# Kernel tuning notes

Hardware: AMD Instinct MI355X
Metric: run time of the kernel (lower is better)

The kernel has to match this reference:

```python
import jax, jax.numpy as jnp
from jax import lax
import numpy as np

B, CG, CY, H, W = 4, 384, 2, 224, 224
CH = 32  # gate / hidden channel count


def conv2d_same(x, w):
    # x: [B,C,H,W], w: [O,I,3,3], stride 1, padding 1, no bias
    return lax.conv_general_dilated(x, w, (1, 1), ((1, 1), (1, 1)),
                                    dimension_numbers=("NCHW", "OIHW", "NCHW"))


def norm_gates(g1, g2, g3):
    # torch: normalize by sum_abs only where sum_abs >= 1, else keep raw gates.
    # Equivalent to dividing by max(sum_abs, 1).
    denom = jnp.maximum(jnp.abs(g1) + jnp.abs(g2) + jnp.abs(g3), 1.0)
    return g1 / denom, g2 / denom, g3 / denom


def propagate(x, g1, g2, g3, horizontal, reverse):
    # GateRecurrent2dnoind: serial scan along W (horizontal) or H (vertical).
    # h(t) = (1 - g1 - g2 - g3) * x(t) + g1*h_prev(i-1) + g2*h_prev(i) + g3*h_prev(i+1)
    ax = 3 if horizontal else 2

    def prep(a):
        a = jnp.flip(a, ax) if reverse else a
        return jnp.moveaxis(a, ax, 0)  # [T, B, C, S]

    xs = (prep(x), prep(g1), prep(g2), prep(g3))

    def step(h, inp):
        xt, a1, a2, a3 = inp
        hu = jnp.pad(h, ((0, 0), (0, 0), (1, 0)))[:, :, :-1]  # neighbor i-1
        hd = jnp.pad(h, ((0, 0), (0, 0), (0, 1)))[:, :, 1:]   # neighbor i+1
        h = (1.0 - a1 - a2 - a3) * xt + a1 * hu + a2 * h + a3 * hd
        return h, h

    h0 = jnp.zeros(xs[0].shape[1:], x.dtype)
    _, ys = lax.scan(step, h0, xs)
    out = jnp.moveaxis(ys, 0, ax)
    return jnp.flip(out, ax) if reverse else out


def spn_net(gates, y):
    # gates: [B,384,H,W] -> 4 directions x 3 gate maps of 32 channels each
    def g(i):
        return gates[:, i * CH:(i + 1) * CH]

    # flags replicated exactly from the source: lr=(T,F), rl=(F,T), du=(F,F), ud=(T,T)
    ylr = propagate(y, *norm_gates(g(0), g(1), g(2)), horizontal=True, reverse=False)
    yrl = propagate(y, *norm_gates(g(3), g(4), g(5)), horizontal=False, reverse=True)
    ydu = propagate(y, *norm_gates(g(6), g(7), g(8)), horizontal=False, reverse=False)
    yud = propagate(y, *norm_gates(g(9), g(10), g(11)), horizontal=True, reverse=True)
    return jnp.maximum(jnp.maximum(ylr, yrl), jnp.maximum(yud, ydu))


def setup_inputs() -> dict:
    key = jax.random.key(0)
    k1, k2, k3, k4 = jax.random.split(key, 4)
    return {
        "out": jax.random.normal(k1, (B, CG, H, W), dtype=jnp.float32),
        "y": jax.random.normal(k2, (B, CY, H, W), dtype=jnp.float32),
        "w3": jax.random.normal(k3, (CH, CY, 3, 3), dtype=jnp.float32) * 0.05,
        "w4": jax.random.normal(k4, (CY, CH, 3, 3), dtype=jnp.float32) * 0.05,
    }


def reference(out, y, w3, w4):
    y32 = conv2d_same(y, w3)          # conv_end_3: 2 -> 32
    y1 = spn_net(out, y32)            # y = self.spnNet(x, y)
    x = spn_net(out, y1)              # x = self.spnNet(x, y)
    x = conv2d_same(x, w4)            # conv_end_4: 32 -> 2
    return jax.nn.log_softmax(x, axis=1)  # nn.LogSoftmax legacy dim=1 on 4D
```

## Files before the change

kernel.cpp:

```cpp
#include <hip/hip_runtime.h>
#include <math.h>

#define HW2 50176
#define NPLANE 6422528

__global__ __launch_bounds__(256) void conv3_kernel(const float* __restrict__ y,
                                                    const float* __restrict__ w3,
                                                    float* __restrict__ y32)
{
    int idx = blockIdx.x * 256 + threadIdx.x;
    if (idx >= NPLANE) return;
    int w  = idx % 224;
    int h  = (idx / 224) % 224;
    int co = (idx / HW2) % 32;
    int b  = idx / (HW2 * 32);
    const float* yb = y + (size_t)b * 2 * HW2;
    float acc = 0.f;
#pragma unroll
    for (int ci = 0; ci < 2; ci++) {
#pragma unroll
        for (int kh = 0; kh < 3; kh++) {
            int hy = h + kh - 1;
            if (hy < 0 || hy > 223) continue;
#pragma unroll
            for (int kw = 0; kw < 3; kw++) {
                int wy = w + kw - 1;
                if (wy < 0 || wy > 223) continue;
                acc += yb[ci * HW2 + hy * 224 + wy] * w3[((co * 2 + ci) * 3 + kh) * 3 + kw];
            }
        }
    }
    y32[idx] = acc;
}

__device__ __forceinline__ float gstep(float a1, float a2, float a3, float xv,
                                       float hu, float hc, float hd)
{
    float den = fabsf(a1) + fabsf(a2) + fabsf(a3);
    den = fmaxf(den, 1.0f);
    return xv + (a1 * (hu - xv) + a2 * (hc - xv) + a3 * (hd - xv)) / den;
}

template <bool REV>
__device__ void scan_vert(const float* __restrict__ g1, const float* __restrict__ g2,
                          const float* __restrict__ g3, const float* __restrict__ xp,
                          float* __restrict__ op, int s, float* hA, float* hB)
{
    int off = (REV ? 223 * 224 : 0) + s;
    float a1 = g1[off], a2 = g2[off], a3 = g3[off], xv = xp[off];
    float* hp = hA;
    float* hn = hB;
    for (int i = 0; i < 224; i++) {
        int offn = off + (REV ? -224 : 224);
        float b1 = 0.f, b2 = 0.f, b3 = 0.f, bx = 0.f;
        if (i < 223) { b1 = g1[offn]; b2 = g2[offn]; b3 = g3[offn]; bx = xp[offn]; }
        float hv = gstep(a1, a2, a3, xv, hp[s], hp[s + 1], hp[s + 2]);
        hn[s + 1] = hv;
        op[off] = hv;
        __syncthreads();
        float* t = hp; hp = hn; hn = t;
        a1 = b1; a2 = b2; a3 = b3; xv = bx;
        off = offn;
    }
}

template <bool REV>
__device__ void scan_horiz(const float* __restrict__ g1, const float* __restrict__ g2,
                           const float* __restrict__ g3, const float* __restrict__ xp,
                           float* __restrict__ op, int s, float* hA, float* hB)
{
    const float* r1 = g1 + s * 224;
    const float* r2 = g2 + s * 224;
    const float* r3 = g3 + s * 224;
    const float* rx = xp + s * 224;
    float* orow = op + s * 224;

    float c1[16], c2[16], c3[16], cx[16];
    float n1[16], n2[16], n3[16], nx[16];

    auto ld = [](float* dst, const float* src, int w0) {
#pragma unroll
        for (int k = 0; k < 4; k++)
            *(float4*)&dst[4 * k] = *(const float4*)&src[w0 + 4 * k];
    };

    int w0 = REV ? 208 : 0;
    ld(c1, r1, w0); ld(c2, r2, w0); ld(c3, r3, w0); ld(cx, rx, w0);

    float* hp = hA;
    float* hn = hB;
    for (int ch = 0; ch < 14; ch++) {
        int w0n = REV ? w0 - 16 : w0 + 16;
        if (ch < 13) { ld(n1, r1, w0n); ld(n2, r2, w0n); ld(n3, r3, w0n); ld(nx, rx, w0n); }
        float ov[16];
#pragma unroll
        for (int j = 0; j < 16; j++) {
            const int k = REV ? 15 - j : j;
            float hv = gstep(c1[k], c2[k], c3[k], cx[k], hp[s], hp[s + 1], hp[s + 2]);
            hn[s + 1] = hv;
            ov[k] = hv;
            __syncthreads();
            float* t = hp; hp = hn; hn = t;
        }
#pragma unroll
        for (int k = 0; k < 4; k++)
            *(float4*)&orow[w0 + 4 * k] = *(float4*)&ov[4 * k];
        if (ch < 13) {
#pragma unroll
            for (int k = 0; k < 16; k++) { c1[k] = n1[k]; c2[k] = n2[k]; c3[k] = n3[k]; cx[k] = nx[k]; }
            w0 = w0n;
        }
    }
}

__global__ __launch_bounds__(224) void scan_kernel(const float* __restrict__ gates,
                                                   const float* __restrict__ x,
                                                   float* __restrict__ dout)
{
    __shared__ float hA[226];
    __shared__ float hB[226];
    int bid = blockIdx.x;
    int d = bid >> 7;
    int b = (bid >> 5) & 3;
    int c = bid & 31;
    int s = threadIdx.x;

    hA[s + 1] = 0.f;
    if (s == 0) { hA[0] = 0.f; hA[225] = 0.f; hB[0] = 0.f; hB[225] = 0.f; }
    __syncthreads();

    const float* g1 = gates + (size_t)(b * 384 + (3 * d) * 32 + c) * HW2;
    const float* g2 = g1 + 32 * (size_t)HW2;
    const float* g3 = g2 + 32 * (size_t)HW2;
    const float* xp = x + (size_t)(b * 32 + c) * HW2;
    float* op = dout + (size_t)d * NPLANE + (size_t)(b * 32 + c) * HW2;

    if (d == 0)      scan_horiz<false>(g1, g2, g3, xp, op, s, hA, hB);
    else if (d == 1) scan_vert<true >(g1, g2, g3, xp, op, s, hA, hB);
    else if (d == 2) scan_vert<false>(g1, g2, g3, xp, op, s, hA, hB);
    else             scan_horiz<true >(g1, g2, g3, xp, op, s, hA, hB);
}

__global__ __launch_bounds__(256) void max4_kernel(const float* __restrict__ D,
                                                   float* __restrict__ o)
{
    const int NP4 = NPLANE / 4;
    int idx = blockIdx.x * 256 + threadIdx.x;
    if (idx >= NP4) return;
    const float4* d0 = (const float4*)D;
    const float4* d1 = d0 + NP4;
    const float4* d2 = d1 + NP4;
    const float4* d3 = d2 + NP4;
    float4 a = d0[idx], b = d1[idx], c = d2[idx], d = d3[idx];
    float4 r;
    r.x = fmaxf(fmaxf(a.x, b.x), fmaxf(c.x, d.x));
    r.y = fmaxf(fmaxf(a.y, b.y), fmaxf(c.y, d.y));
    r.z = fmaxf(fmaxf(a.z, b.z), fmaxf(c.z, d.z));
    r.w = fmaxf(fmaxf(a.w, b.w), fmaxf(c.w, d.w));
    ((float4*)o)[idx] = r;
}

__global__ __launch_bounds__(256) void conv4ls_kernel(const float* __restrict__ x,
                                                      const float* __restrict__ w4,
                                                      float* __restrict__ out)
{
    __shared__ float wsh[576];
    for (int i = threadIdx.x; i < 576; i += 256) wsh[i] = w4[i];
    __syncthreads();
    int idx = blockIdx.x * 256 + threadIdx.x;
    if (idx >= 4 * HW2) return;
    int w = idx % 224;
    int h = (idx / 224) % 224;
    int b = idx / HW2;
    const float* xb = x + (size_t)b * 32 * HW2;
    float acc0 = 0.f, acc1 = 0.f;
    for (int ci = 0; ci < 32; ci++) {
        const float* xc = xb + ci * HW2;
#pragma unroll
        for (int kh = 0; kh < 3; kh++) {
            int hy = h + kh - 1;
            if (hy < 0 || hy > 223) continue;
#pragma unroll
            for (int kw = 0; kw < 3; kw++) {
                int wy = w + kw - 1;
                if (wy < 0 || wy > 223) continue;
                float v = xc[hy * 224 + wy];
                acc0 += v * wsh[(ci * 3 + kh) * 3 + kw];
                acc1 += v * wsh[288 + (ci * 3 + kh) * 3 + kw];
            }
        }
    }
    float m = fmaxf(acc0, acc1);
    float l = m + logf(expf(acc0 - m) + expf(acc1 - m));
    out[(size_t)(b * 2) * HW2 + h * 224 + w]     = acc0 - l;
    out[(size_t)(b * 2 + 1) * HW2 + h * 224 + w] = acc1 - l;
}

extern "C" void kernel_launch(void* const* d_in, const int* in_sizes, int n_in,
                              void* d_out, int out_size, void* d_ws, size_t ws_size,
                              hipStream_t stream)
{
    const float* gates = (const float*)d_in[0];
    const float* y     = (const float*)d_in[1];
    const float* w3    = (const float*)d_in[2];
    const float* w4    = (const float*)d_in[3];
    float* out = (float*)d_out;
    float* ws  = (float*)d_ws;

    float* y32 = ws;
    float* D   = ws + NPLANE;

    conv3_kernel<<<NPLANE / 256, 256, 0, stream>>>(y, w3, y32);
    scan_kernel<<<512, 224, 0, stream>>>(gates, y32, D);
    max4_kernel<<<NPLANE / 4 / 256, 256, 0, stream>>>(D, y32);
    scan_kernel<<<512, 224, 0, stream>>>(gates, y32, D);
    max4_kernel<<<NPLANE / 4 / 256, 256, 0, stream>>>(D, y32);
    conv4ls_kernel<<<(4 * HW2) / 256, 256, 0, stream>>>(y32, w4, out);
}
```

Baseline: 902.9 us.

## Run each scan plane in one wavefront with register-blocked lanes and shuffles

Each scan plane is now handled by a single 64-lane wavefront instead of a 224-thread block. Each lane owns four adjacent scan positions in registers and exchanges boundary values with its neighbours through warp shuffles, which removes the shared-memory ping-pong and the __syncthreads at every step. Loads are double-buffered float4 tiles, gate loads use nontemporal hints, and the division becomes a hardware reciprocal followed by an FMA. In exchange, only 512 small one-wave blocks are launched, which limits occupancy and latency hiding, and the approximate reciprocal can change results slightly.

```diff
diff --git a/kernel.cpp b/kernel.cpp
--- a/kernel.cpp
+++ b/kernel.cpp
@@ -3,6 +3,8 @@
 
 #define HW2 50176
 #define NPLANE 6422528
+
+typedef float f4 __attribute__((ext_vector_type(4)));
 
 __global__ __launch_bounds__(256) void conv3_kernel(const float* __restrict__ y,
                                                     const float* __restrict__ w3,
@@ -36,109 +38,183 @@
 __device__ __forceinline__ float gstep(float a1, float a2, float a3, float xv,
                                        float hu, float hc, float hd)
 {
-    float den = fabsf(a1) + fabsf(a2) + fabsf(a3);
-    den = fmaxf(den, 1.0f);
-    return xv + (a1 * (hu - xv) + a2 * (hc - xv) + a3 * (hd - xv)) / den;
-}
-
-template <bool REV>
-__device__ void scan_vert(const float* __restrict__ g1, const float* __restrict__ g2,
-                          const float* __restrict__ g3, const float* __restrict__ xp,
-                          float* __restrict__ op, int s, float* hA, float* hB)
-{
-    int off = (REV ? 223 * 224 : 0) + s;
-    float a1 = g1[off], a2 = g2[off], a3 = g3[off], xv = xp[off];
-    float* hp = hA;
-    float* hn = hB;
-    for (int i = 0; i < 224; i++) {
-        int offn = off + (REV ? -224 : 224);
-        float b1 = 0.f, b2 = 0.f, b3 = 0.f, bx = 0.f;
-        if (i < 223) { b1 = g1[offn]; b2 = g2[offn]; b3 = g3[offn]; bx = xp[offn]; }
-        float hv = gstep(a1, a2, a3, xv, hp[s], hp[s + 1], hp[s + 2]);
-        hn[s + 1] = hv;
-        op[off] = hv;
-        __syncthreads();
-        float* t = hp; hp = hn; hn = t;
-        a1 = b1; a2 = b2; a3 = b3; xv = bx;
-        off = offn;
-    }
-}
-
-template <bool REV>
-__device__ void scan_horiz(const float* __restrict__ g1, const float* __restrict__ g2,
-                           const float* __restrict__ g3, const float* __restrict__ xp,
-                           float* __restrict__ op, int s, float* hA, float* hB)
-{
-    const float* r1 = g1 + s * 224;
-    const float* r2 = g2 + s * 224;
-    const float* r3 = g3 + s * 224;
-    const float* rx = xp + s * 224;
-    float* orow = op + s * 224;
-
-    float c1[16], c2[16], c3[16], cx[16];
-    float n1[16], n2[16], n3[16], nx[16];
-
-    auto ld = [](float* dst, const float* src, int w0) {
-#pragma unroll
-        for (int k = 0; k < 4; k++)
-            *(float4*)&dst[4 * k] = *(const float4*)&src[w0 + 4 * k];
-    };
-
-    int w0 = REV ? 208 : 0;
-    ld(c1, r1, w0); ld(c2, r2, w0); ld(c3, r3, w0); ld(cx, rx, w0);
-
-    float* hp = hA;
-    float* hn = hB;
-    for (int ch = 0; ch < 14; ch++) {
-        int w0n = REV ? w0 - 16 : w0 + 16;
-        if (ch < 13) { ld(n1, r1, w0n); ld(n2, r2, w0n); ld(n3, r3, w0n); ld(nx, rx, w0n); }
-        float ov[16];
-#pragma unroll
-        for (int j = 0; j < 16; j++) {
-            const int k = REV ? 15 - j : j;
-            float hv = gstep(c1[k], c2[k], c3[k], cx[k], hp[s], hp[s + 1], hp[s + 2]);
-            hn[s + 1] = hv;
-            ov[k] = hv;
-            __syncthreads();
-            float* t = hp; hp = hn; hn = t;
-        }
-#pragma unroll
-        for (int k = 0; k < 4; k++)
-            *(float4*)&orow[w0 + 4 * k] = *(float4*)&ov[4 * k];
-        if (ch < 13) {
-#pragma unroll
-            for (int k = 0; k < 16; k++) { c1[k] = n1[k]; c2[k] = n2[k]; c3[k] = n3[k]; cx[k] = nx[k]; }
-            w0 = w0n;
-        }
-    }
-}
-
-__global__ __launch_bounds__(224) void scan_kernel(const float* __restrict__ gates,
-                                                   const float* __restrict__ x,
-                                                   float* __restrict__ dout)
-{
-    __shared__ float hA[226];
-    __shared__ float hB[226];
+    float den = fmaxf(fabsf(a1) + fabsf(a2) + fabsf(a3), 1.0f);
+    float r = __builtin_amdgcn_rcpf(den);
+    float t = a1 * (hu - xv) + a2 * (hc - xv) + a3 * (hd - xv);
+    return fmaf(t, r, xv);
+}
+
+
+template <bool REV>
+__device__ __forceinline__ void vload(f4& d1, f4& d2, f4& d3, f4 dx[1],
+                                      const float* __restrict__ g1, const float* __restrict__ g2,
+                                      const float* __restrict__ g3, const float* __restrict__ xp,
+                                      int i, int col, bool act)
+{
+    int r = REV ? 223 - i : i;
+    int off = r * 224 + col;
+    if (act) {
+        d1 = __builtin_nontemporal_load((const f4*)&g1[off]);
+        d2 = __builtin_nontemporal_load((const f4*)&g2[off]);
+        d3 = __builtin_nontemporal_load((const f4*)&g3[off]);
+        dx[0] = *(const f4*)&xp[off];
+    } else {
+        d1 = (f4)0.f; d2 = (f4)0.f; d3 = (f4)0.f; dx[0] = (f4)0.f;
+    }
+}
+
+template <bool REV>
+__device__ __forceinline__ void vload4(f4 d1[4], f4 d2[4], f4 d3[4], f4 dx[4],
+                                       const float* __restrict__ g1, const float* __restrict__ g2,
+                                       const float* __restrict__ g3, const float* __restrict__ xp,
+                                       int cc, int col, bool act)
+{
+#pragma unroll
+    for (int j = 0; j < 4; j++)
+        vload<REV>(d1[j], d2[j], d3[j], &dx[j], g1, g2, g3, xp, 4 * cc + j, col, act);
+}
+
+template <bool REV>
+__device__ __forceinline__ void vcomp(const f4 b1[4], const f4 b2[4],
+                                      const f4 b3[4], const f4 bx[4],
+                                      float& h0, float& h1, float& h2, float& h3,
+                                      float* __restrict__ op, int cc, int col,
+                                      bool act, int lane)
+{
+#pragma unroll
+    for (int j = 0; j < 4; j++) {
+        float up = __shfl_up(h3, 1);
+        if (lane == 0) up = 0.f;
+        float dn = __shfl_down(h0, 1);
+        float t0 = gstep(b1[j].x, b2[j].x, b3[j].x, bx[j].x, up, h0, h1);
+        float t1 = gstep(b1[j].y, b2[j].y, b3[j].y, bx[j].y, h0, h1, h2);
+        float t2 = gstep(b1[j].z, b2[j].z, b3[j].z, bx[j].z, h1, h2, h3);
+        float t3 = gstep(b1[j].w, b2[j].w, b3[j].w, bx[j].w, h2, h3, dn);
+        h0 = t0; h1 = t1; h2 = t2; h3 = t3;
+        if (act) {
+            int i = 4 * cc + j;
+            int r = REV ? 223 - i : i;
+            f4 o; o.x = h0; o.y = h1; o.z = h2; o.w = h3;
+            *(f4*)&op[r * 224 + col] = o;
+        }
+    }
+}
+
+template <bool REV>
+__device__ void scan_v(const float* __restrict__ g1, const float* __restrict__ g2,
+                       const float* __restrict__ g3, const float* __restrict__ xp,
+                       float* __restrict__ op, int lane)
+{
+    const bool act = lane < 56;
+    const int col = 4 * lane;
+    float h0 = 0.f, h1 = 0.f, h2 = 0.f, h3 = 0.f;
+    f4 A1[4], A2[4], A3[4], Ax[4];
+    f4 B1[4], B2[4], B3[4], Bx[4];
+
+    vload4<REV>(A1, A2, A3, Ax, g1, g2, g3, xp, 0, col, act);
+#pragma unroll 1
+    for (int cc = 0; cc < 56; cc += 2) {
+        vload4<REV>(B1, B2, B3, Bx, g1, g2, g3, xp, cc + 1, col, act);
+        vcomp<REV>(A1, A2, A3, Ax, h0, h1, h2, h3, op, cc, col, act, lane);
+        if (cc + 2 < 56)
+            vload4<REV>(A1, A2, A3, Ax, g1, g2, g3, xp, cc + 2, col, act);
+        vcomp<REV>(B1, B2, B3, Bx, h0, h1, h2, h3, op, cc + 1, col, act, lane);
+    }
+}
+
+template <bool REV>
+__device__ __forceinline__ void hload(f4 d1[4], f4 d2[4], f4 d3[4], f4 dx[4],
+                                      const float* __restrict__ g1, const float* __restrict__ g2,
+                                      const float* __restrict__ g3, const float* __restrict__ xp,
+                                      int cc, int r0, bool act)
+{
+    int w0 = REV ? 220 - 4 * cc : 4 * cc;
+#pragma unroll
+    for (int rr = 0; rr < 4; rr++) {
+        int off = (r0 + rr) * 224 + w0;
+        if (act) {
+            d1[rr] = __builtin_nontemporal_load((const f4*)&g1[off]);
+            d2[rr] = __builtin_nontemporal_load((const f4*)&g2[off]);
+            d3[rr] = __builtin_nontemporal_load((const f4*)&g3[off]);
+            dx[rr] = *(const f4*)&xp[off];
+        } else {
+            d1[rr] = (f4)0.f; d2[rr] = (f4)0.f; d3[rr] = (f4)0.f; dx[rr] = (f4)0.f;
+        }
+    }
+}
+
+template <bool REV>
+__device__ __forceinline__ void hcomp(const f4 b1[4], const f4 b2[4],
+                                      const f4 b3[4], const f4 bx[4],
+                                      float& h0, float& h1, float& h2, float& h3,
+                                      float* __restrict__ op, int cc, int r0,
+                                      bool act, int lane)
+{
+    f4 o[4];
+#pragma unroll
+    for (int j = 0; j < 4; j++) {
+        const int e = REV ? 3 - j : j;
+        float up = __shfl_up(h3, 1);
+        if (lane == 0) up = 0.f;
+        float dn = __shfl_down(h0, 1);
+        float t0 = gstep(b1[0][e], b2[0][e], b3[0][e], bx[0][e], up, h0, h1);
+        float t1 = gstep(b1[1][e], b2[1][e], b3[1][e], bx[1][e], h0, h1, h2);
+        float t2 = gstep(b1[2][e], b2[2][e], b3[2][e], bx[2][e], h1, h2, h3);
+        float t3 = gstep(b1[3][e], b2[3][e], b3[3][e], bx[3][e], h2, h3, dn);
+        h0 = t0; h1 = t1; h2 = t2; h3 = t3;
+        o[0][e] = t0; o[1][e] = t1; o[2][e] = t2; o[3][e] = t3;
+    }
+    if (act) {
+        int w0 = REV ? 220 - 4 * cc : 4 * cc;
+#pragma unroll
+        for (int rr = 0; rr < 4; rr++)
+            *(f4*)&op[(r0 + rr) * 224 + w0] = o[rr];
+    }
+}
+
+template <bool REV>
+__device__ void scan_h(const float* __restrict__ g1, const float* __restrict__ g2,
+                       const float* __restrict__ g3, const float* __restrict__ xp,
+                       float* __restrict__ op, int lane)
+{
+    const bool act = lane < 56;
+    const int r0 = 4 * lane;
+    float h0 = 0.f, h1 = 0.f, h2 = 0.f, h3 = 0.f;
+    f4 A1[4], A2[4], A3[4], Ax[4];
+    f4 B1[4], B2[4], B3[4], Bx[4];
+
+    hload<REV>(A1, A2, A3, Ax, g1, g2, g3, xp, 0, r0, act);
+#pragma unroll 1
+    for (int cc = 0; cc < 56; cc += 2) {
+        hload<REV>(B1, B2, B3, Bx, g1, g2, g3, xp, cc + 1, r0, act);
+        hcomp<REV>(A1, A2, A3, Ax, h0, h1, h2, h3, op, cc, r0, act, lane);
+        if (cc + 2 < 56)
+            hload<REV>(A1, A2, A3, Ax, g1, g2, g3, xp, cc + 2, r0, act);
+        hcomp<REV>(B1, B2, B3, Bx, h0, h1, h2, h3, op, cc + 1, r0, act, lane);
+    }
+}
+
+__global__ __launch_bounds__(64) void scan_kernel(const float* __restrict__ gates,
+                                                  const float* __restrict__ x,
+                                                  float* __restrict__ D)
+{
     int bid = blockIdx.x;
-    int d = bid >> 7;
-    int b = (bid >> 5) & 3;
-    int c = bid & 31;
-    int s = threadIdx.x;
-
-    hA[s + 1] = 0.f;
-    if (s == 0) { hA[0] = 0.f; hA[225] = 0.f; hB[0] = 0.f; hB[225] = 0.f; }
-    __syncthreads();
-
-    const float* g1 = gates + (size_t)(b * 384 + (3 * d) * 32 + c) * HW2;
+    int d = bid & 3;
+    int p = bid >> 2;
+    int b = p >> 5;
+    int c = p & 31;
+    int lane = threadIdx.x;
+
+    const float* g1 = gates + (size_t)(b * 384 + 3 * d * 32 + c) * HW2;
     const float* g2 = g1 + 32 * (size_t)HW2;
     const float* g3 = g2 + 32 * (size_t)HW2;
     const float* xp = x + (size_t)(b * 32 + c) * HW2;
-    float* op = dout + (size_t)d * NPLANE + (size_t)(b * 32 + c) * HW2;
-
-    if (d == 0)      scan_horiz<false>(g1, g2, g3, xp, op, s, hA, hB);
-    else if (d == 1) scan_vert<true >(g1, g2, g3, xp, op, s, hA, hB);
-    else if (d == 2) scan_vert<false>(g1, g2, g3, xp, op, s, hA, hB);
-    else             scan_horiz<true >(g1, g2, g3, xp, op, s, hA, hB);
+    float* op = D + (size_t)d * NPLANE + (size_t)(b * 32 + c) * HW2;
+
+    if (d == 0)      scan_h<false>(g1, g2, g3, xp, op, lane);
+    else if (d == 1) scan_v<true >(g1, g2, g3, xp, op, lane);
+    else if (d == 2) scan_v<false>(g1, g2, g3, xp, op, lane);
+    else             scan_h<true >(g1, g2, g3, xp, op, lane);
 }
 
 __global__ __launch_bounds__(256) void max4_kernel(const float* __restrict__ D,
@@ -147,17 +223,17 @@
     const int NP4 = NPLANE / 4;
     int idx = blockIdx.x * 256 + threadIdx.x;
     if (idx >= NP4) return;
-    const float4* d0 = (const float4*)D;
-    const float4* d1 = d0 + NP4;
-    const float4* d2 = d1 + NP4;
-    const float4* d3 = d2 + NP4;
-    float4 a = d0[idx], b = d1[idx], c = d2[idx], d = d3[idx];
-    float4 r;
+    const f4* d0 = (const f4*)D;
+    const f4* d1 = d0 + NP4;
+    const f4* d2 = d1 + NP4;
+    const f4* d3 = d2 + NP4;
+    f4 a = d0[idx], b = d1[idx], c = d2[idx], d = d3[idx];
+    f4 r;
     r.x = fmaxf(fmaxf(a.x, b.x), fmaxf(c.x, d.x));
     r.y = fmaxf(fmaxf(a.y, b.y), fmaxf(c.y, d.y));
     r.z = fmaxf(fmaxf(a.z, b.z), fmaxf(c.z, d.z));
     r.w = fmaxf(fmaxf(a.w, b.w), fmaxf(c.w, d.w));
-    ((float4*)o)[idx] = r;
+    ((f4*)o)[idx] = r;
 }
 
 __global__ __launch_bounds__(256) void conv4ls_kernel(const float* __restrict__ x,
@@ -211,9 +287,9 @@
     float* D   = ws + NPLANE;
 
     conv3_kernel<<<NPLANE / 256, 256, 0, stream>>>(y, w3, y32);
-    scan_kernel<<<512, 224, 0, stream>>>(gates, y32, D);
+    scan_kernel<<<512, 64, 0, stream>>>(gates, y32, D);
     max4_kernel<<<NPLANE / 4 / 256, 256, 0, stream>>>(D, y32);
-    scan_kernel<<<512, 224, 0, stream>>>(gates, y32, D);
+    scan_kernel<<<512, 64, 0, stream>>>(gates, y32, D);
     max4_kernel<<<NPLANE / 4 / 256, 256, 0, stream>>>(D, y32);
     conv4ls_kernel<<<(4 * HW2) / 256, 256, 0, stream>>>(y32, w4, out);
 }
```

New measurement: 1.254 ms. 1.39x slower.
